# Kernel tuning notes

Measured on AMD Instinct MI355X. Metric: run time of the kernel, lower is better.

## Reference

```python
import jax, jax.numpy as jnp
import numpy as np

V = 25; NE = 5; DIM = 192; H = 6; HD = 32; N = 64; T = 64
SCALE = HD ** -0.5
COEFF = 0.4
NTU_EDGES = [(1,2),(2,21),(3,21),(4,3),(5,21),(6,5),(7,6),(8,7),(9,21),(10,9),(11,10),(12,11),(13,1),(14,13),(15,14),(16,15),(17,1),(18,17),(19,18),(20,19),(22,23),(23,8),(24,25),(25,12)]

def _compute_hops():
    # replicate MHSA.__init__ hop-distance computation (A = [I, adj, adj] summed+binarized)
    adj = np.zeros((V, V))
    for i, j in NTU_EDGES:
        adj[i-1, j-1] = 1.0; adj[j-1, i-1] = 1.0
    h1 = ((np.eye(V) + adj) != 0).astype(np.float64)
    h = [None] * V
    h[0] = np.eye(V); h[1] = h1
    hops = np.zeros((V, V))
    for i in range(2, V):
        h[i] = ((h[i-1] @ h1.T) != 0).astype(np.float64)
    for i in range(V-1, 0, -1):
        if np.any(h[i] - h[i-1]):
            h[i] = h[i] - h[i-1]
            hops += i * h[i]
    return hops.astype(np.int32)

def setup_inputs() -> dict:
    key = jax.random.key(0)
    ks = jax.random.split(key, 12)
    hops = jnp.asarray(_compute_hops())
    n_hop = int(hops.max()) + 1
    std = 0.02
    return {
        "x": jax.random.normal(ks[0], (N, DIM, T, V), jnp.float32),
        "joint_label": jnp.arange(V, dtype=jnp.int32) % NE,  # all 5 hyperedge labels present
        "groups": NE,  # unused by forward (kept for signature fidelity)
        "he_weight": jax.random.uniform(ks[1], (NE,), jnp.float32),
        "hops": hops,
        "ln_g": jnp.ones((DIM,), jnp.float32),
        "ln_b": jnp.zeros((DIM,), jnp.float32),
        "hgc_w": std * jax.random.normal(ks[2], (DIM, DIM), jnp.float32),
        "q_w": std * jax.random.normal(ks[3], (DIM, DIM), jnp.float32),
        "kv_w": std * jax.random.normal(ks[4], (2 * DIM, DIM), jnp.float32),
        "proj_w": std * jax.random.normal(ks[5], (DIM, HD), jnp.float32),  # grouped 1x1 conv, groups=6
        "proj_b": jnp.zeros((DIM,), jnp.float32),
        "rpe": std * jax.random.normal(ks[6], (n_hop, DIM), jnp.float32),
        "w1": std * jax.random.normal(ks[7], (H, HD), jnp.float32),
        "outer": jnp.tile(jnp.eye(V, dtype=jnp.float32), (H, 1, 1)) + std * jax.random.normal(ks[8], (H, V, V), jnp.float32),
        "alpha": 0.1 * jnp.ones((1,), jnp.float32),
        "lin1_w": std * jax.random.normal(ks[9], (T // 5, T), jnp.float32),
        "lin1_b": jnp.zeros((T // 5,), jnp.float32),
        "lin2_w": std * jax.random.normal(ks[10], (T, T // 5), jnp.float32),
        "lin2_b": jnp.zeros((T,), jnp.float32),
    }

def _forward(x, joint_label, he_weight, hops, ln_g, ln_b, hgc_w, q_w, kv_w, proj_w, proj_b, rpe, w1, outer, alpha, lin1_w, lin1_b, lin2_w, lin2_b):
    N_, C, T_, V_ = x.shape
    # ---- HGattn branch: hypergraph conv + temporal squeeze-excite gate ----
    label = jax.nn.one_hot(joint_label, NE, dtype=x.dtype)            # (V, 5)
    label1 = label / label.sum(0, keepdims=True)
    label1 = label1 / jnp.sqrt(label.sum(1, keepdims=True))
    label1 = (he_weight[None, :] * label1).T                          # (5, V)
    norm_label = label / label.sum(1, keepdims=True)
    h_adj = norm_label @ label1                                       # (V, V)
    z = jnp.einsum('nctv,vw->nctw', x, h_adj)
    op = jnp.einsum('nctv,oc->notv', z, hgc_w)                        # (N, dim, T, V) 1x1 conv
    op_tr = op.transpose(0, 1, 3, 2)                                  # (N, dim, V, T)
    s = op_tr.mean(axis=(1, 2))                                       # (N, T) global avg pool over (dim, V)
    g = jax.nn.sigmoid(jax.nn.relu(s @ lin1_w.T + lin1_b) @ lin2_w.T + lin2_b)  # (N, T)
    op_final = op_tr + COEFF * (op_tr * g[:, None, None, :])
    e = op_final.transpose(0, 1, 3, 2)                                # (N, dim, T, V)
    # ---- LayerNorm over channel dim ----
    xc = x.transpose(0, 2, 3, 1)                                      # (N, T, V, C)
    mu = xc.mean(-1, keepdims=True)
    var = xc.var(-1, keepdims=True)
    xn = (((xc - mu) / jnp.sqrt(var + 1e-5)) * ln_g + ln_b).transpose(0, 3, 1, 2)
    # ---- MHSA with hop-indexed relative bias, e-branch scores, outer fusion ----
    q = jnp.einsum('nctv,oc->notv', xn, q_w).reshape(N_, H, HD, T_, V_).transpose(0, 3, 1, 4, 2)   # (N,T,H,V,hd)
    kv = jnp.einsum('nctv,oc->notv', xn, kv_w).reshape(N_, 2, H, HD, T_, V_)
    k = kv[:, 0].transpose(0, 3, 1, 4, 2)
    v = kv[:, 1].transpose(0, 3, 1, 4, 2)
    e_k = e.reshape(N_, H, HD, T_, V_).transpose(0, 3, 1, 4, 2)
    k_r = rpe[hops].reshape(V_, V_, H, HD)                            # hop-distance relative position table
    b = jnp.einsum('bthnc,nmhc->bthnm', q, k_r)
    c = jnp.einsum('bthnc,bthmc->bthnm', q, e_k)
    d = jnp.einsum('hc,bthmc->bthm', w1, e_k)[..., None, :]
    a = jnp.einsum('bthnc,bthmc->bthnm', q, k)
    attn = jax.nn.softmax((a + b + c + d) * SCALE, axis=-1)
    o = jnp.einsum('bthnm,bthmc->bthnc', alpha * attn + outer[None, None], v)
    o = o.transpose(0, 1, 2, 4, 3).reshape(N_, T_, DIM, V_).transpose(0, 2, 1, 3)  # (N, dim, T, V)
    # grouped 1x1 conv projection (groups = H)
    og = o.reshape(N_, H, HD, T_, V_)
    wg = proj_w.reshape(H, HD, HD)
    o = jnp.einsum('ngitv,goi->ngotv', og, wg).reshape(N_, DIM, T_, V_) + proj_b[None, :, None, None]
    return x + o  # dim_in == dim -> identity skip

def reference(x, joint_label, groups, he_weight, hops, ln_g, ln_b, hgc_w, q_w, kv_w, proj_w, proj_b, rpe, w1, outer, alpha, lin1_w, lin1_b, lin2_w, lin2_b):
    return _forward(x, joint_label, he_weight, hops, ln_g, ln_b, hgc_w, q_w, kv_w, proj_w, proj_b, rpe, w1, outer, alpha, lin1_w, lin1_b, lin2_w, lin2_b)
```

## Files before the change

### kernel.cpp

```cpp
#include <hip/hip_runtime.h>
#include <hip/hip_bf16.h>

using bf16 = __hip_bfloat16;
typedef __bf16 bf16x8 __attribute__((ext_vector_type(8)));
typedef float f32x4 __attribute__((ext_vector_type(4)));

constexpr int kDim = 192;
constexpr int kH = 6;
constexpr int kHd = 32;
constexpr int kN = 64;
constexpr int kT = 64;
constexpr int kV = 25;
constexpr int kP = kT * kV;
constexpr int kNCstride = kDim * kP;
constexpr float kScale = 0.17677669529663687f;
constexpr float kCoeff = 0.4f;

__global__ void __launch_bounds__(256) setup_kernel(
    const int* __restrict__ jl, const float* __restrict__ hew,
    const float* __restrict__ hgc, const float* __restrict__ qw,
    const float* __restrict__ kvw, const float* __restrict__ rpe,
    const float* __restrict__ proj_w, const float* __restrict__ lng,
    const float* __restrict__ lnb, int n_hop, float* __restrict__ hadj,
    bf16* __restrict__ Wb, float* __restrict__ G, float* __restrict__ Bb,
    bf16* __restrict__ RPEb, bf16* __restrict__ pwb, bf16* __restrict__ VT) {
  const int bid = blockIdx.x;
  const int tid = threadIdx.x;
  if (bid < 576) {
    int i = bid * 256 + tid;
    float v;
    if (i < 36864) {
      v = hgc[i];
    } else {
      int local = i - 36864;
      int c = local % kDim;
      v = (local < 36864) ? qw[local] : kvw[local - 36864];
      v *= lng[c];
    }
    Wb[i] = __float2bfloat16(v);
  } else if (bid == 576) {
    __shared__ int lbl[kV];
    __shared__ int cnt[8];
    if (tid < 8) cnt[tid] = 0;
    __syncthreads();
    if (tid < kV) { lbl[tid] = jl[tid]; atomicAdd(&cnt[lbl[tid]], 1); }
    __syncthreads();
    for (int idx = tid; idx < kV * kV; idx += 256) {
      int v = idx / kV, w = idx - v * kV;
      float val = 0.f;
      if (lbl[v] == lbl[w]) val = hew[lbl[v]] / (float)cnt[lbl[v]];
      hadj[idx] = val;
    }
  } else if (bid == 577) {
    for (int i = tid; i < kH * 16 * kHd; i += 256) {
      int h = i >> 9, hp = (i >> 5) & 15, d = i & 31;
      float v = (hp < n_hop) ? rpe[hp * kDim + h * kHd + d] : 0.f;
      RPEb[i] = __float2bfloat16(v);
    }
    for (int i = tid; i < kDim * kHd; i += 256)
      pwb[i] = __float2bfloat16(proj_w[i]);
  } else if (bid < 722) {
    int o = (bid - 578) * 4 + (tid >> 6);
    int lane = tid & 63;
    const float* Wr =
        (o < kDim) ? (qw + (size_t)o * kDim) : (kvw + (size_t)(o - kDim) * kDim);
    float gs = 0.f, bs = 0.f;
    for (int c = lane; c < kDim; c += 64) {
      float wv = Wr[c];
      gs += wv * lng[c];
      bs += wv * lnb[c];
    }
    for (int off = 32; off > 0; off >>= 1) {
      gs += __shfl_down(gs, off);
      bs += __shfl_down(bs, off);
    }
    if (lane == 0) { G[o] = gs; Bb[o] = bs; }
  } else {
    int row = (bid - 722) * 256 + tid;
    if (row < kN * kT * kDim) {
      uint4 z = {0u, 0u, 0u, 0u};
      *reinterpret_cast<uint4*>(reinterpret_cast<char*>(VT) + (size_t)row * 64 +
                                48) = z;
    }
  }
}

__global__ void __launch_bounds__(256) prep_kernel(
    const float* __restrict__ x, bf16* __restrict__ XR, float* __restrict__ mu,
    float* __restrict__ rstd) {
  __shared__ float ps[kV][25], ps2[kV][25];
  const int tid = threadIdx.x;
  const int t = blockIdx.x, n = blockIdx.y;
  const float* xb = x + (size_t)n * kNCstride + t * kV;
  size_t ob = ((size_t)n * kP + t * kV) * kDim;
  for (int idx = tid; idx < 600; idx += 256) {
    int p = idx % 25, c8 = idx / 25;
    float a = 0.f, b = 0.f;
    union { uint4 u; __bf16 h[8]; } pk;
#pragma unroll
    for (int i = 0; i < 8; ++i) {
      float v = xb[(size_t)(c8 * 8 + i) * kP + p];
      a += v;
      b += v * v;
      pk.h[i] = (__bf16)v;
    }
    *reinterpret_cast<uint4*>(XR + ob + (size_t)p * kDim + c8 * 8) = pk.u;
    ps[p][c8] = a;
    ps2[p][c8] = b;
  }
  __syncthreads();
  if (tid < kV) {
    float a = 0.f, b = 0.f;
#pragma unroll
    for (int c8 = 0; c8 < 24; ++c8) { a += ps[tid][c8]; b += ps2[tid][c8]; }
    float m = a * (1.f / kDim);
    float var = b * (1.f / kDim) - m * m;
    int gid = n * kP + t * kV + tid;
    mu[gid] = m;
    rstd[gid] = rsqrtf(var + 1e-5f);
  }
}

template <int OBN, int MOUT, bool VS, bool LNF>
__global__ void __launch_bounds__(64) mfma_gemm_kernel(
    const bf16* __restrict__ A, const bf16* __restrict__ B,
    bf16* __restrict__ out, bf16* __restrict__ VT,
    const float* __restrict__ muA, const float* __restrict__ rsA,
    const float* __restrict__ G, const float* __restrict__ Bb) {
  int id = blockIdx.x;
  int per = gridDim.x >> 3;
  int wg = (id & 7) * per + (id >> 3);
  int n = wg / (25 * OBN);
  int rem = wg - n * (25 * OBN);
  const int pb = (rem / OBN) * 64;
  const int ob = (rem % OBN) * 64;
  const int l = threadIdx.x;
  B += (size_t)n * kNCstride;
  out += (size_t)n * kP * MOUT;
  f32x4 acc[4][4] = {};
  const int lm = l & 15;
  const int lk = (l >> 4) * 8;
  for (int kb = 0; kb < kDim; kb += 32) {
    bf16x8 af[4], bfv[4];
#pragma unroll
    for (int mf = 0; mf < 4; ++mf)
      af[mf] = *reinterpret_cast<const bf16x8*>(
          A + (size_t)(ob + mf * 16 + lm) * kDim + kb + lk);
#pragma unroll
    for (int nf = 0; nf < 4; ++nf)
      bfv[nf] = *reinterpret_cast<const bf16x8*>(
          B + (size_t)(pb + nf * 16 + lm) * kDim + kb + lk);
#pragma unroll
    for (int mf = 0; mf < 4; ++mf)
#pragma unroll
      for (int nf = 0; nf < 4; ++nf)
        acc[mf][nf] = __builtin_amdgcn_mfma_f32_16x16x32_bf16(
            af[mf], bfv[nf], acc[mf][nf], 0, 0, 0);
  }
  const int r0 = (l >> 4) * 4;
  float rsv[4], muv[4];
  if (LNF) {
#pragma unroll
    for (int nf = 0; nf < 4; ++nf) {
      int p = pb + nf * 16 + lm;
      rsv[nf] = rsA[n * kP + p];
      muv[nf] = muA[n * kP + p];
    }
  }
  int tt[4], vv[4];
#pragma unroll
  for (int nf = 0; nf < 4; ++nf) {
    int p = pb + nf * 16 + lm;
    tt[nf] = p / 25;
    vv[nf] = p - tt[nf] * 25;
  }
#pragma unroll
  for (int mf = 0; mf < 4; ++mf) {
    const int o0 = ob + mf * 16 + r0;
    float ga[4] = {0.f, 0.f, 0.f, 0.f}, ba[4] = {0.f, 0.f, 0.f, 0.f};
    if (LNF) {
      float4 g4 = *reinterpret_cast<const float4*>(G + o0);
      float4 b4 = *reinterpret_cast<const float4*>(Bb + o0);
      ga[0] = g4.x; ga[1] = g4.y; ga[2] = g4.z; ga[3] = g4.w;
      ba[0] = b4.x; ba[1] = b4.y; ba[2] = b4.z; ba[3] = b4.w;
    }
    if (!VS || o0 < 384) {
#pragma unroll
      for (int nf = 0; nf < 4; ++nf) {
        const int p = pb + nf * 16 + lm;
        union { uint2 u; bf16 b[4]; } pk;
#pragma unroll
        for (int r = 0; r < 4; ++r) {
          float vvv = acc[mf][nf][r];
          if (LNF) vvv = rsv[nf] * (vvv - muv[nf] * ga[r]) + ba[r];
          pk.b[r] = __float2bfloat16(vvv);
        }
        *reinterpret_cast<uint2*>(out + (size_t)p * MOUT + o0) = pk.u;
      }
    } else {
#pragma unroll
      for (int nf = 0; nf < 4; ++nf) {
        size_t rowb =
            ((size_t)(n * kT + tt[nf]) * kDim + (o0 - 384)) * 32 + vv[nf];
#pragma unroll
        for (int r = 0; r < 4; ++r) {
          float vvv = acc[mf][nf][r];
          if (LNF) vvv = rsv[nf] * (vvv - muv[nf] * ga[r]) + ba[r];
          VT[rowb + (size_t)r * 32] = __float2bfloat16(vvv);
        }
      }
    }
  }
}

__global__ void __launch_bounds__(256) haapply_kernel(
    bf16* __restrict__ OP, const float* __restrict__ hadjg,
    float* __restrict__ s_out) {
  __shared__ ushort tile[kV * kDim];
  __shared__ float ha[640];
  __shared__ float red[4];
  const int tid = threadIdx.x;
  const int t = blockIdx.x, n = blockIdx.y;
  size_t base = ((size_t)n * kP + t * kV) * kDim;
  for (int i = tid; i < kV * kV; i += 256) ha[i] = hadjg[i];
  const uint2* src = reinterpret_cast<const uint2*>(OP + base);
  uint2* dst2 = reinterpret_cast<uint2*>(tile);
  for (int i = tid; i < kV * kDim / 4; i += 256) dst2[i] = src[i];
  __syncthreads();
  float ssum = 0.f;
  for (int idx = tid; idx < 600; idx += 256) {
    int c8 = idx % 24, w = idx / 24;
    float acc[8] = {0.f, 0.f, 0.f, 0.f, 0.f, 0.f, 0.f, 0.f};
    for (int v = 0; v < kV; ++v) {
      float coef = ha[v * kV + w];
      union { uint4 u; __bf16 h[8]; } ld;
      ld.u = *reinterpret_cast<const uint4*>(tile + v * kDim + c8 * 8);
#pragma unroll
      for (int j = 0; j < 8; ++j) acc[j] += coef * (float)ld.h[j];
    }
    union { uint4 u; __bf16 h[8]; } pk;
    float s8 = 0.f;
#pragma unroll
    for (int j = 0; j < 8; ++j) { pk.h[j] = (__bf16)acc[j]; s8 += acc[j]; }
    *reinterpret_cast<uint4*>(OP + base + (size_t)w * kDim + c8 * 8) = pk.u;
    ssum += s8;
  }
  for (int off = 32; off > 0; off >>= 1) ssum += __shfl_down(ssum, off);
  if ((tid & 63) == 0) red[tid >> 6] = ssum;
  __syncthreads();
  if (tid == 0)
    s_out[n * kT + t] = (red[0] + red[1] + red[2] + red[3]) *
                        (1.f / (float)(kDim * kV));
}

__global__ void gate_kernel(const float* __restrict__ s,
                            const float* __restrict__ w1l,
                            const float* __restrict__ b1,
                            const float* __restrict__ w2l,
                            const float* __restrict__ b2,
                            float* __restrict__ gatef) {
  __shared__ float sh[kT];
  __shared__ float hid[12];
  int n = blockIdx.x, t = threadIdx.x;
  sh[t] = s[n * kT + t];
  __syncthreads();
  if (t < 12) {
    float a = b1[t];
    for (int j = 0; j < kT; ++j) a += sh[j] * w1l[t * kT + j];
    hid[t] = fmaxf(a, 0.f);
  }
  __syncthreads();
  float a = b2[t];
  for (int j = 0; j < 12; ++j) a += hid[j] * w2l[t * 12 + j];
  float g = 1.f / (1.f + __expf(-a));
  gatef[n * kT + t] = 1.f + kCoeff * g;
}

__global__ void __launch_bounds__(384) attn_kernel(
    const bf16* __restrict__ QK, const bf16* __restrict__ VT,
    const bf16* __restrict__ OP, const float* __restrict__ gatef,
    const int* __restrict__ hops, const bf16* __restrict__ RPEb,
    const float* __restrict__ w1, const float* __restrict__ outer,
    const float* __restrict__ alpha_p, const bf16* __restrict__ pwb,
    const float* __restrict__ proj_b, const float* __restrict__ x,
    float* __restrict__ out) {
  __shared__ ushort wls[kH][2304];
  __shared__ unsigned char hopsB[kV][32];
  const int tid = threadIdx.x;
  const int lane = tid & 63;
  const int h = tid >> 6;
  const int t = blockIdx.x, n = blockIdx.y;
  const int nt = n * kT + t;
  const int lm = lane & 15, g = lane >> 4;
  const bool w1ok = (lm + 16) < kV;

  for (int i = tid; i < kV * 32; i += 384) {
    int v = i >> 5, w = i & 31;
    hopsB[v][w] = (w < kV) ? (unsigned char)hops[v * kV + w] : 0;
  }
  __syncthreads();

  bf16* Pp = (bf16*)&wls[h][0];
  bf16* OLp = (bf16*)&wls[h][1152];
  float* QRp = (float*)&wls[h][1152];

  const float f = gatef[nt];
  const float alpha = alpha_p[0];
  const bf16* Qbase = QK + (size_t)(nt * kV) * 384;
  const bf16* Ebase = OP + (size_t)(nt * kV) * kDim;
  const int colO = h * kHd + g * 8;

  bf16x8 qf[2], kf[2], ef[2];
#pragma unroll
  for (int mf = 0; mf < 2; ++mf) {
    const bf16* row = Qbase + (size_t)(mf * 16 + lm) * 384;
    qf[mf] = *reinterpret_cast<const bf16x8*>(row + colO);
    kf[mf] = *reinterpret_cast<const bf16x8*>(row + kDim + colO);
    ef[mf] = *reinterpret_cast<const bf16x8*>(
        Ebase + (size_t)(mf * 16 + lm) * kDim + colO);
  }
  bf16x8 rf = *reinterpret_cast<const bf16x8*>(RPEb + (h * 16 + lm) * kHd + g * 8);

  float w1v[8];
  {
    float4 wa = *reinterpret_cast<const float4*>(w1 + h * kHd + g * 8);
    float4 wb = *reinterpret_cast<const float4*>(w1 + h * kHd + g * 8 + 4);
    w1v[0] = wa.x; w1v[1] = wa.y; w1v[2] = wa.z; w1v[3] = wa.w;
    w1v[4] = wb.x; w1v[5] = wb.y; w1v[6] = wb.z; w1v[7] = wb.w;
  }
  float dt[2];
#pragma unroll
  for (int nf = 0; nf < 2; ++nf) {
    float a = 0.f;
#pragma unroll
    for (int j = 0; j < 8; ++j) a += w1v[j] * (float)ef[nf][j];
    a += __shfl_xor(a, 16);
    a += __shfl_xor(a, 32);
    dt[nf] = f * a;
  }

  bf16x8 kef[2];
#pragma unroll
  for (int nf = 0; nf < 2; ++nf)
#pragma unroll
    for (int j = 0; j < 8; ++j)
      kef[nf][j] = (__bf16)((float)kf[nf][j] + f * (float)ef[nf][j]);

  f32x4 aK[2][2] = {};
  f32x4 aR[2] = {};
#pragma unroll
  for (int mf = 0; mf < 2; ++mf) {
#pragma unroll
    for (int nf = 0; nf < 2; ++nf)
      aK[mf][nf] =
          __builtin_amdgcn_mfma_f32_16x16x32_bf16(qf[mf], kef[nf], aK[mf][nf], 0, 0, 0);
    aR[mf] = __builtin_amdgcn_mfma_f32_16x16x32_bf16(qf[mf], rf, aR[mf], 0, 0, 0);
  }

#pragma unroll
  for (int mf = 0; mf < 2; ++mf)
#pragma unroll
    for (int r = 0; r < 4; ++r)
      QRp[(mf * 16 + g * 4 + r) * 17 + lm] = aR[mf][r];

#pragma unroll
  for (int mf = 0; mf < 2; ++mf) {
#pragma unroll
    for (int r = 0; r < 4; ++r) {
      int v = mf * 16 + g * 4 + r;
      int vc = v < kV ? v : kV - 1;
      int hp0 = hopsB[vc][lm];
      int hp1 = hopsB[vc][lm + 16];
      float s0 = (aK[mf][0][r] + QRp[v * 17 + hp0] + dt[0]) * kScale;
      float s1 = (aK[mf][1][r] + QRp[v * 17 + hp1] + dt[1]) * kScale;
      if (!w1ok) s1 = -3.0e38f;
      float m = fmaxf(s0, s1);
#pragma unroll
      for (int d = 1; d < 16; d <<= 1) m = fmaxf(m, __shfl_xor(m, d));
      float e0 = __expf(s0 - m);
      float e1 = w1ok ? __expf(s1 - m) : 0.f;
      float sum = e0 + e1;
#pragma unroll
      for (int d = 1; d < 16; d <<= 1) sum += __shfl_xor(sum, d);
      float inv = alpha / sum;
      float o0 = outer[h * (kV * kV) + vc * kV + lm];
      float o1 = w1ok ? outer[h * (kV * kV) + vc * kV + lm + 16] : 0.f;
      Pp[v * 36 + lm] = __float2bfloat16(e0 * inv + o0);
      Pp[v * 36 + lm + 16] = __float2bfloat16(w1ok ? e1 * inv + o1 : 0.f);
    }
  }

  bf16x8 pa[2], vb[2];
#pragma unroll
  for (int mf = 0; mf < 2; ++mf)
    pa[mf] = *reinterpret_cast<const bf16x8*>(Pp + (mf * 16 + lm) * 36 + g * 8);
#pragma unroll
  for (int nf = 0; nf < 2; ++nf)
    vb[nf] = *reinterpret_cast<const bf16x8*>(
        VT + ((size_t)(nt * kDim + h * kHd + nf * 16 + lm)) * 32 + g * 8);
  f32x4 aO[2][2] = {};
#pragma unroll
  for (int mf = 0; mf < 2; ++mf)
#pragma unroll
    for (int nf = 0; nf < 2; ++nf)
      aO[mf][nf] =
          __builtin_amdgcn_mfma_f32_16x16x32_bf16(pa[mf], vb[nf], aO[mf][nf], 0, 0, 0);

#pragma unroll
  for (int mf = 0; mf < 2; ++mf)
#pragma unroll
    for (int nf = 0; nf < 2; ++nf)
#pragma unroll
      for (int r = 0; r < 4; ++r)
        OLp[(mf * 16 + g * 4 + r) * 36 + nf * 16 + lm] =
            __float2bfloat16(aO[mf][nf][r]);

  bf16x8 oa[2], pwf[2];
#pragma unroll
  for (int nf = 0; nf < 2; ++nf)
    oa[nf] = *reinterpret_cast<const bf16x8*>(OLp + (nf * 16 + lm) * 36 + g * 8);
#pragma unroll
  for (int mf = 0; mf < 2; ++mf)
    pwf[mf] = *reinterpret_cast<const bf16x8*>(pwb +
        (h * kHd + mf * 16 + lm) * kHd + g * 8);
  f32x4 aF[2][2] = {};
#pragma unroll
  for (int mf = 0; mf < 2; ++mf)
#pragma unroll
    for (int nf = 0; nf < 2; ++nf)
      aF[mf][nf] =
          __builtin_amdgcn_mfma_f32_16x16x32_bf16(pwf[mf], oa[nf], aF[mf][nf], 0, 0, 0);

#pragma unroll
  for (int mf = 0; mf < 2; ++mf) {
#pragma unroll
    for (int r = 0; r < 4; ++r) {
      int oo = mf * 16 + g * 4 + r;
      int c = h * kHd + oo;
      float pbv = proj_b[c];
      size_t gbase = (size_t)n * kNCstride + (size_t)c * kP + t * kV;
#pragma unroll
      for (int nf = 0; nf < 2; ++nf) {
        int v = nf * 16 + lm;
        if (v < kV) out[gbase + v] = x[gbase + v] + aF[mf][nf][r] + pbv;
      }
    }
  }
}

extern "C" void kernel_launch(void* const* d_in, const int* in_sizes, int n_in,
                              void* d_out, int out_size, void* d_ws,
                              size_t ws_size, hipStream_t stream) {
  const float* x = (const float*)d_in[0];
  const int* joint_label = (const int*)d_in[1];
  const float* he_weight = (const float*)d_in[3];
  const int* hops = (const int*)d_in[4];
  const float* ln_g = (const float*)d_in[5];
  const float* ln_b = (const float*)d_in[6];
  const float* hgc_w = (const float*)d_in[7];
  const float* q_w = (const float*)d_in[8];
  const float* kv_w = (const float*)d_in[9];
  const float* proj_w = (const float*)d_in[10];
  const float* proj_b = (const float*)d_in[11];
  const float* rpe = (const float*)d_in[12];
  const float* w1 = (const float*)d_in[13];
  const float* outer = (const float*)d_in[14];
  const float* alpha = (const float*)d_in[15];
  const float* lin1_w = (const float*)d_in[16];
  const float* lin1_b = (const float*)d_in[17];
  const float* lin2_w = (const float*)d_in[18];
  const float* lin2_b = (const float*)d_in[19];
  const int n_hop = in_sizes[12] / kDim;

  char* w = (char*)d_ws;
  bf16* QK = (bf16*)w;
  w += (size_t)kN * kP * 2 * kDim * 2;
  bf16* XR = (bf16*)w;
  w += (size_t)kN * kP * kDim * 2;
  bf16* OP = (bf16*)w;
  w += (size_t)kN * kP * kDim * 2;
  w += 65536;
  bf16* VT = (bf16*)w;
  w += (size_t)kN * kT * kDim * 32 * 2;
  bf16* Wb = (bf16*)w;
  w += (size_t)768 * kDim * 2;
  bf16* RPEb = (bf16*)w;
  w += (size_t)kH * 16 * kHd * 2;
  bf16* pwb = (bf16*)w;
  w += (size_t)kDim * kHd * 2;
  float* hadj = (float*)w;
  w += 1024 * 4;
  float* s_ws = (float*)w;
  w += kN * kT * 4;
  float* gatef = (float*)w;
  w += kN * kT * 4;
  float* mu = (float*)w;
  w += (size_t)kN * kP * 4;
  float* rstd = (float*)w;
  w += (size_t)kN * kP * 4;
  float* G = (float*)w;
  w += 576 * 4;
  float* Bb = (float*)w;
  w += 576 * 4;

  hipLaunchKernelGGL(setup_kernel, dim3(3794), dim3(256), 0, stream,
                     joint_label, he_weight, hgc_w, q_w, kv_w, rpe, proj_w,
                     ln_g, ln_b, n_hop, hadj, Wb, G, Bb, RPEb, pwb, VT);
  hipLaunchKernelGGL(prep_kernel, dim3(kT, kN), dim3(256), 0, stream, x, XR,
                     mu, rstd);
  hipLaunchKernelGGL((mfma_gemm_kernel<3, kDim, false, false>),
                     dim3(25 * 3 * kN), dim3(64), 0, stream, Wb, XR, OP,
                     (bf16*)nullptr, nullptr, nullptr, nullptr, nullptr);
  hipLaunchKernelGGL(haapply_kernel, dim3(kT, kN), dim3(256), 0, stream, OP,
                     hadj, s_ws);
  hipLaunchKernelGGL(gate_kernel, dim3(kN), dim3(kT), 0, stream, s_ws, lin1_w,
                     lin1_b, lin2_w, lin2_b, gatef);
  hipLaunchKernelGGL((mfma_gemm_kernel<9, 384, true, true>),
                     dim3(25 * 9 * kN), dim3(64), 0, stream, Wb + 192 * kDim,
                     XR, QK, VT, mu, rstd, G, Bb);
  hipLaunchKernelGGL(attn_kernel, dim3(kT, kN), dim3(384), 0, stream, QK, VT,
                     OP, gatef, hops, RPEb, w1, outer, alpha, pwb, proj_b, x,
                     (float*)d_out);
}
```

Measured before the change: 343.1 us.

## Merge hypergraph and QKV GEMMs into one launch; use shuffles for RPE lookup

The two separate MFMA GEMM launches (hypergraph projection and the LayerNorm-folded Q/K/V projection) become one kernel with 12 output tiles per pixel block. Each block branches on its tile index to pick the epilogue, so the shared XR tile is read within a single grid and one launch disappears. In the attention kernel, the hop table staging in shared memory, its barrier and the QR spill to LDS are replaced by direct global hop reads plus cross-lane shuffles of the RPE scores. The V and projection-weight loads are also hoisted earlier to overlap with compute. The cost is extra branch divergence across blocks and uncached per-lane hop loads.

```diff
diff --git a/kernel.cpp b/kernel.cpp
--- a/kernel.cpp
+++ b/kernel.cpp
@@ -121,22 +121,21 @@
   }
 }
 
-template <int OBN, int MOUT, bool VS, bool LNF>
-__global__ void __launch_bounds__(64) mfma_gemm_kernel(
+__global__ void __launch_bounds__(64) gemm_all_kernel(
     const bf16* __restrict__ A, const bf16* __restrict__ B,
-    bf16* __restrict__ out, bf16* __restrict__ VT,
+    bf16* __restrict__ OP, bf16* __restrict__ QK, bf16* __restrict__ VT,
     const float* __restrict__ muA, const float* __restrict__ rsA,
     const float* __restrict__ G, const float* __restrict__ Bb) {
   int id = blockIdx.x;
   int per = gridDim.x >> 3;
   int wg = (id & 7) * per + (id >> 3);
-  int n = wg / (25 * OBN);
-  int rem = wg - n * (25 * OBN);
-  const int pb = (rem / OBN) * 64;
-  const int ob = (rem % OBN) * 64;
+  int n = wg / 300;
+  int rem = wg - n * 300;
+  const int pt = rem / 12;
+  const int ob = rem % 12;
+  const int pb = pt * 64;
   const int l = threadIdx.x;
   B += (size_t)n * kNCstride;
-  out += (size_t)n * kP * MOUT;
   f32x4 acc[4][4] = {};
   const int lm = l & 15;
   const int lk = (l >> 4) * 8;
@@ -145,7 +144,7 @@
 #pragma unroll
     for (int mf = 0; mf < 4; ++mf)
       af[mf] = *reinterpret_cast<const bf16x8*>(
-          A + (size_t)(ob + mf * 16 + lm) * kDim + kb + lk);
+          A + (size_t)(ob * 64 + mf * 16 + lm) * kDim + kb + lk);
 #pragma unroll
     for (int nf = 0; nf < 4; ++nf)
       bfv[nf] = *reinterpret_cast<const bf16x8*>(
@@ -158,54 +157,58 @@
             af[mf], bfv[nf], acc[mf][nf], 0, 0, 0);
   }
   const int r0 = (l >> 4) * 4;
-  float rsv[4], muv[4];
-  if (LNF) {
-#pragma unroll
-    for (int nf = 0; nf < 4; ++nf) {
-      int p = pb + nf * 16 + lm;
-      rsv[nf] = rsA[n * kP + p];
-      muv[nf] = muA[n * kP + p];
-    }
-  }
-  int tt[4], vv[4];
-#pragma unroll
-  for (int nf = 0; nf < 4; ++nf) {
-    int p = pb + nf * 16 + lm;
-    tt[nf] = p / 25;
-    vv[nf] = p - tt[nf] * 25;
-  }
-#pragma unroll
-  for (int mf = 0; mf < 4; ++mf) {
-    const int o0 = ob + mf * 16 + r0;
-    float ga[4] = {0.f, 0.f, 0.f, 0.f}, ba[4] = {0.f, 0.f, 0.f, 0.f};
-    if (LNF) {
-      float4 g4 = *reinterpret_cast<const float4*>(G + o0);
-      float4 b4 = *reinterpret_cast<const float4*>(Bb + o0);
-      ga[0] = g4.x; ga[1] = g4.y; ga[2] = g4.z; ga[3] = g4.w;
-      ba[0] = b4.x; ba[1] = b4.y; ba[2] = b4.z; ba[3] = b4.w;
-    }
-    if (!VS || o0 < 384) {
+  if (ob < 3) {
+    OP += (size_t)n * kP * kDim;
+#pragma unroll
+    for (int mf = 0; mf < 4; ++mf) {
+      const int o0 = ob * 64 + mf * 16 + r0;
 #pragma unroll
       for (int nf = 0; nf < 4; ++nf) {
         const int p = pb + nf * 16 + lm;
         union { uint2 u; bf16 b[4]; } pk;
 #pragma unroll
-        for (int r = 0; r < 4; ++r) {
-          float vvv = acc[mf][nf][r];
-          if (LNF) vvv = rsv[nf] * (vvv - muv[nf] * ga[r]) + ba[r];
-          pk.b[r] = __float2bfloat16(vvv);
-        }
-        *reinterpret_cast<uint2*>(out + (size_t)p * MOUT + o0) = pk.u;
+        for (int r = 0; r < 4; ++r) pk.b[r] = __float2bfloat16(acc[mf][nf][r]);
+        *reinterpret_cast<uint2*>(OP + (size_t)p * kDim + o0) = pk.u;
+      }
+    }
+    return;
+  }
+  float rsv[4], muv[4];
+  int tt[4], vv[4];
+#pragma unroll
+  for (int nf = 0; nf < 4; ++nf) {
+    int p = pb + nf * 16 + lm;
+    rsv[nf] = rsA[n * kP + p];
+    muv[nf] = muA[n * kP + p];
+    tt[nf] = p / 25;
+    vv[nf] = p - tt[nf] * 25;
+  }
+#pragma unroll
+  for (int mf = 0; mf < 4; ++mf) {
+    const int oq = ob * 64 - 192 + mf * 16 + r0;
+    float4 g4 = *reinterpret_cast<const float4*>(G + oq);
+    float4 b4 = *reinterpret_cast<const float4*>(Bb + oq);
+    float ga[4] = {g4.x, g4.y, g4.z, g4.w};
+    float ba[4] = {b4.x, b4.y, b4.z, b4.w};
+    if (ob < 9) {
+#pragma unroll
+      for (int nf = 0; nf < 4; ++nf) {
+        const int p = pb + nf * 16 + lm;
+        union { uint2 u; bf16 b[4]; } pk;
+#pragma unroll
+        for (int r = 0; r < 4; ++r)
+          pk.b[r] = __float2bfloat16(
+              rsv[nf] * (acc[mf][nf][r] - muv[nf] * ga[r]) + ba[r]);
+        *reinterpret_cast<uint2*>(QK + ((size_t)n * kP + p) * 384 + oq) = pk.u;
       }
     } else {
 #pragma unroll
       for (int nf = 0; nf < 4; ++nf) {
         size_t rowb =
-            ((size_t)(n * kT + tt[nf]) * kDim + (o0 - 384)) * 32 + vv[nf];
+            ((size_t)(n * kT + tt[nf]) * kDim + (oq - 384)) * 32 + vv[nf];
 #pragma unroll
         for (int r = 0; r < 4; ++r) {
-          float vvv = acc[mf][nf][r];
-          if (LNF) vvv = rsv[nf] * (vvv - muv[nf] * ga[r]) + ba[r];
+          float vvv = rsv[nf] * (acc[mf][nf][r] - muv[nf] * ga[r]) + ba[r];
           VT[rowb + (size_t)r * 32] = __float2bfloat16(vvv);
         }
       }
@@ -285,7 +288,6 @@
     const float* __restrict__ proj_b, const float* __restrict__ x,
     float* __restrict__ out) {
   __shared__ ushort wls[kH][2304];
-  __shared__ unsigned char hopsB[kV][32];
   const int tid = threadIdx.x;
   const int lane = tid & 63;
   const int h = tid >> 6;
@@ -294,15 +296,8 @@
   const int lm = lane & 15, g = lane >> 4;
   const bool w1ok = (lm + 16) < kV;
 
-  for (int i = tid; i < kV * 32; i += 384) {
-    int v = i >> 5, w = i & 31;
-    hopsB[v][w] = (w < kV) ? (unsigned char)hops[v * kV + w] : 0;
-  }
-  __syncthreads();
-
   bf16* Pp = (bf16*)&wls[h][0];
   bf16* OLp = (bf16*)&wls[h][1152];
-  float* QRp = (float*)&wls[h][1152];
 
   const float f = gatef[nt];
   const float alpha = alpha_p[0];
@@ -320,6 +315,14 @@
         Ebase + (size_t)(mf * 16 + lm) * kDim + colO);
   }
   bf16x8 rf = *reinterpret_cast<const bf16x8*>(RPEb + (h * 16 + lm) * kHd + g * 8);
+  bf16x8 vb[2], pwf[2];
+#pragma unroll
+  for (int nf = 0; nf < 2; ++nf) {
+    vb[nf] = *reinterpret_cast<const bf16x8*>(
+        VT + ((size_t)(nt * kDim + h * kHd + nf * 16 + lm)) * 32 + g * 8);
+    pwf[nf] = *reinterpret_cast<const bf16x8*>(
+        pwb + (h * kHd + nf * 16 + lm) * kHd + g * 8);
+  }
 
   float w1v[8];
   {
@@ -358,21 +361,17 @@
   }
 
 #pragma unroll
-  for (int mf = 0; mf < 2; ++mf)
-#pragma unroll
-    for (int r = 0; r < 4; ++r)
-      QRp[(mf * 16 + g * 4 + r) * 17 + lm] = aR[mf][r];
-
-#pragma unroll
   for (int mf = 0; mf < 2; ++mf) {
 #pragma unroll
     for (int r = 0; r < 4; ++r) {
       int v = mf * 16 + g * 4 + r;
       int vc = v < kV ? v : kV - 1;
-      int hp0 = hopsB[vc][lm];
-      int hp1 = hopsB[vc][lm + 16];
-      float s0 = (aK[mf][0][r] + QRp[v * 17 + hp0] + dt[0]) * kScale;
-      float s1 = (aK[mf][1][r] + QRp[v * 17 + hp1] + dt[1]) * kScale;
+      int hp0 = hops[vc * kV + lm];
+      int hp1 = w1ok ? hops[vc * kV + lm + 16] : 0;
+      float qr0 = __shfl(aR[mf][r], g * 16 + hp0);
+      float qr1 = __shfl(aR[mf][r], g * 16 + hp1);
+      float s0 = (aK[mf][0][r] + qr0 + dt[0]) * kScale;
+      float s1 = (aK[mf][1][r] + qr1 + dt[1]) * kScale;
       if (!w1ok) s1 = -3.0e38f;
       float m = fmaxf(s0, s1);
 #pragma unroll
@@ -390,14 +389,10 @@
     }
   }
 
-  bf16x8 pa[2], vb[2];
+  bf16x8 pa[2];
 #pragma unroll
   for (int mf = 0; mf < 2; ++mf)
     pa[mf] = *reinterpret_cast<const bf16x8*>(Pp + (mf * 16 + lm) * 36 + g * 8);
-#pragma unroll
-  for (int nf = 0; nf < 2; ++nf)
-    vb[nf] = *reinterpret_cast<const bf16x8*>(
-        VT + ((size_t)(nt * kDim + h * kHd + nf * 16 + lm)) * 32 + g * 8);
   f32x4 aO[2][2] = {};
 #pragma unroll
   for (int mf = 0; mf < 2; ++mf)
@@ -415,14 +410,10 @@
         OLp[(mf * 16 + g * 4 + r) * 36 + nf * 16 + lm] =
             __float2bfloat16(aO[mf][nf][r]);
 
-  bf16x8 oa[2], pwf[2];
+  bf16x8 oa[2];
 #pragma unroll
   for (int nf = 0; nf < 2; ++nf)
     oa[nf] = *reinterpret_cast<const bf16x8*>(OLp + (nf * 16 + lm) * 36 + g * 8);
-#pragma unroll
-  for (int mf = 0; mf < 2; ++mf)
-    pwf[mf] = *reinterpret_cast<const bf16x8*>(pwb +
-        (h * kHd + mf * 16 + lm) * kHd + g * 8);
   f32x4 aF[2][2] = {};
 #pragma unroll
   for (int mf = 0; mf < 2; ++mf)
@@ -508,16 +499,12 @@
                      ln_g, ln_b, n_hop, hadj, Wb, G, Bb, RPEb, pwb, VT);
   hipLaunchKernelGGL(prep_kernel, dim3(kT, kN), dim3(256), 0, stream, x, XR,
                      mu, rstd);
-  hipLaunchKernelGGL((mfma_gemm_kernel<3, kDim, false, false>),
-                     dim3(25 * 3 * kN), dim3(64), 0, stream, Wb, XR, OP,
-                     (bf16*)nullptr, nullptr, nullptr, nullptr, nullptr);
+  hipLaunchKernelGGL(gemm_all_kernel, dim3(25 * 12 * kN), dim3(64), 0, stream,
+                     Wb, XR, OP, QK, VT, mu, rstd, G, Bb);
   hipLaunchKernelGGL(haapply_kernel, dim3(kT, kN), dim3(256), 0, stream, OP,
                      hadj, s_ws);
   hipLaunchKernelGGL(gate_kernel, dim3(kN), dim3(kT), 0, stream, s_ws, lin1_w,
                      lin1_b, lin2_w, lin2_b, gatef);
-  hipLaunchKernelGGL((mfma_gemm_kernel<9, 384, true, true>),
-                     dim3(25 * 9 * kN), dim3(64), 0, stream, Wb + 192 * kDim,
-                     XR, QK, VT, mu, rstd, G, Bb);
   hipLaunchKernelGGL(attn_kernel, dim3(kT, kN), dim3(384), 0, stream, QK, VT,
                      OP, gatef, hops, RPEb, w1, outer, alpha, pwb, proj_b, x,
                      (float*)d_out);
```

New measurement: 354.0 us. 1.03x slower.
